# Kernel optimization log

Measured on AMD Instinct MI355X. Metric: run time of the kernel, lower is better.

Reference implementation:

```python
import jax, jax.numpy as jnp
import numpy as np

E = 16      # num_experts
K = 4       # num_experts_per_tok
H = 2048    # hidden_size
I = 1408    # moe_intermediate_size
SI = 5632   # shared expert intermediate size
CAP = 1024
NORM_TOPK = False


def setup_inputs() -> dict:
    key = jax.random.key(0)
    ks = jax.random.split(key, 9)
    def w(k, shape, fan_in):
        return jax.random.normal(k, shape, jnp.float32) * (fan_in ** -0.5)
    return {
        "hidden_states": jax.random.normal(ks[0], (1, 2048, H), jnp.float32),
        "gate_w":  w(ks[1], (E, H), H),        # router: Linear(H -> E), no bias
        "we_gate": w(ks[2], (E, I, H), H),     # per-expert gate_proj weights
        "we_up":   w(ks[3], (E, I, H), H),     # per-expert up_proj weights
        "we_down": w(ks[4], (E, H, I), I),     # per-expert down_proj weights
        "ws_gate": w(ks[5], (SI, H), H),       # shared expert gate_proj
        "ws_up":   w(ks[6], (SI, H), H),       # shared expert up_proj
        "ws_down": w(ks[7], (H, SI), SI),      # shared expert down_proj
        "sg_w":    w(ks[8], (1, H), H),        # shared_expert_gate: Linear(H -> 1)
    }


def reference(hidden_states, gate_w, we_gate, we_up, we_down,
              ws_gate, ws_up, ws_down, sg_w):
    B, S, Hd = hidden_states.shape
    x = hidden_states.reshape(-1, Hd)                      # [T, H]
    T = x.shape[0]

    # --- router ---
    router_logits = x @ gate_w.T                           # [T, E]
    probs = jax.nn.softmax(router_logits.astype(jnp.float32), axis=-1)
    topw, topi = jax.lax.top_k(probs, K)                   # [T, K]
    if NORM_TOPK:
        topw = topw / topw.sum(axis=-1, keepdims=True)

    # --- dispatch: flatten (token, slot) assignments ---
    A = T * K
    fe = topi.reshape(A)                                   # expert id per assignment
    fw = topw.reshape(A)                                   # routing weight per assignment
    ft = jnp.repeat(jnp.arange(T), K)                      # token id per assignment
    # position of each assignment within its expert (rank in arrival order)
    oh = jax.nn.one_hot(fe, E, dtype=jnp.int32)            # [A, E]
    pos = jnp.take_along_axis(jnp.cumsum(oh, axis=0) - 1, fe[:, None], axis=1)[:, 0]
    valid = pos < CAP
    # scatter tokens into per-expert buffers; overflow goes to dummy row CAP
    buf = jnp.zeros((E, CAP + 1, Hd), x.dtype)
    buf = buf.at[fe, jnp.where(valid, pos, CAP)].set(x[ft])[:, :CAP]  # [E, C, H]

    # --- per-expert SiLU-gated MLP (batched grouped GEMMs) ---
    g = jnp.einsum('ech,eih->eci', buf, we_gate)
    u = jnp.einsum('ech,eih->eci', buf, we_up)
    eo = jnp.einsum('eci,ehi->ech', jax.nn.silu(g) * u, we_down)      # [E, C, H]

    # --- combine: weighted scatter-add back to tokens ---
    ga = eo[fe, jnp.minimum(pos, CAP - 1)]                 # [A, H]
    wcomb = (fw * valid.astype(fw.dtype)).astype(x.dtype)
    y = jnp.zeros((T, Hd), x.dtype).at[ft].add(ga * wcomb[:, None])

    # --- shared expert with sigmoid gate ---
    sh = (jax.nn.silu(x @ ws_gate.T) * (x @ ws_up.T)) @ ws_down.T
    sh = jax.nn.sigmoid(x @ sg_w.T) * sh

    out = (y + sh).reshape(B, S, Hd)
    return out, router_logits
```

## Files before the change

kernel.cpp:

```cpp
#include <hip/hip_runtime.h>

#define T_TOK 2048
#define NE 16
#define KTOP 4
#define HD 2048
#define ID 1408
#define SID 5632
#define CAPACITY 1024

typedef __attribute__((ext_vector_type(8))) short short8;
typedef __attribute__((ext_vector_type(4))) float floatx4;

__device__ __forceinline__ short f2b(float f){
  union { float f; unsigned u; } v; v.f = f;
  unsigned r = v.u + 0x7fffu + ((v.u >> 16) & 1u);
  return (short)(r >> 16);
}
__device__ __forceinline__ float b2f(short s){
  union { float f; unsigned u; } v; v.u = ((unsigned)(unsigned short)s) << 16;
  return v.f;
}
__device__ __forceinline__ unsigned cvt_pk(float a, float b){
  unsigned r;
  asm("v_cvt_pk_bf16_f32 %0, %1, %2" : "=v"(r) : "v"(a), "v"(b));
  return r;
}
__device__ __forceinline__ short8 cvt8(float4 a, float4 b){
  union { unsigned d[4]; short8 s; } u;
  u.d[0] = cvt_pk(a.x, a.y); u.d[1] = cvt_pk(a.z, a.w);
  u.d[2] = cvt_pk(b.x, b.y); u.d[3] = cvt_pk(b.z, b.w);
  return u.s;
}
__device__ __forceinline__ void gl16(const void* g, void* l){
  __builtin_amdgcn_global_load_lds(
      (const __attribute__((address_space(1))) void*)g,
      (__attribute__((address_space(3))) void*)l, 16, 0, 0);
}

__device__ __forceinline__ void conv_range(
    int cb, int ncb,
    const float* __restrict__ s1, short* __restrict__ d1, long long n1,
    const float* __restrict__ s2, short* __restrict__ d2, long long n2)
{
  const long long tot = n1 + n2;
  const long long stride = (long long)ncb * 256;
  #pragma unroll 2
  for (long long i = (long long)cb * 256 + threadIdx.x; i < tot; i += stride){
    const float* s; short8* d; long long j;
    if (i < n1){ s = s1; d = (short8*)d1; j = i; }
    else       { s = s2; d = (short8*)d2; j = i - n1; }
    float4 f0 = ((const float4*)s)[j * 2];
    float4 f1 = ((const float4*)s)[j * 2 + 1];
    d[j] = cvt8(f0, f1);
  }
}

__global__ void moe_zero(int* __restrict__ counts){
  if (threadIdx.x < NE) counts[threadIdx.x] = 0;
}

__global__ void moe_router(const float* __restrict__ x,
                           const float* __restrict__ gate_w,
                           const float* __restrict__ sg_w,
                           float* __restrict__ logits_out,
                           short* __restrict__ xb,
                           int* __restrict__ counts,
                           int* __restrict__ slot_token,
                           float* __restrict__ slot_w,
                           int* __restrict__ tslot,
                           float* __restrict__ tw,
                           float* __restrict__ sg,
                           const float* cs1, short* cd1, long long cn1,
                           const float* cs2, short* cd2, long long cn2)
{
  if (blockIdx.x >= 512){
    conv_range(blockIdx.x - 512, gridDim.x - 512, cs1, cd1, cn1, cs2, cd2, cn2);
    return;
  }
  int wave = threadIdx.x >> 6, lane = threadIdx.x & 63;
  int t = (blockIdx.x << 2) + wave;
  const float4* xr = (const float4*)(x + (size_t)t * HD);
  short8* xbw = (short8*)(xb + (size_t)t * HD);
  float acc[17];
  #pragma unroll
  for (int e = 0; e < 17; ++e) acc[e] = 0.f;
  #pragma unroll
  for (int j = 0; j < 4; ++j){
    int i4 = (j * 64 + lane) * 2;
    float4 x0 = xr[i4], x1 = xr[i4 + 1];
    xbw[j * 64 + lane] = cvt8(x0, x1);
    #pragma unroll
    for (int e = 0; e < 16; ++e){
      const float4* gr = (const float4*)(gate_w + e * HD);
      float4 g0 = gr[i4], g1 = gr[i4 + 1];
      acc[e] += x0.x*g0.x + x0.y*g0.y + x0.z*g0.z + x0.w*g0.w
              + x1.x*g1.x + x1.y*g1.y + x1.z*g1.z + x1.w*g1.w;
    }
    const float4* sr = (const float4*)sg_w;
    float4 s0 = sr[i4], s1 = sr[i4 + 1];
    acc[16] += x0.x*s0.x + x0.y*s0.y + x0.z*s0.z + x0.w*s0.w
             + x1.x*s1.x + x1.y*s1.y + x1.z*s1.z + x1.w*s1.w;
  }
  #pragma unroll
  for (int e = 0; e < 17; ++e){
    float v = acc[e];
    #pragma unroll
    for (int off = 32; off > 0; off >>= 1) v += __shfl_xor(v, off, 64);
    acc[e] = v;
  }
  if (lane == 0){
    float m = acc[0];
    #pragma unroll
    for (int e = 1; e < 16; ++e) m = fmaxf(m, acc[e]);
    float p[16]; float s = 0.f;
    #pragma unroll
    for (int e = 0; e < 16; ++e){ p[e] = expf(acc[e] - m); s += p[e]; }
    float inv = 1.f / s;
    #pragma unroll
    for (int e = 0; e < 16; ++e) logits_out[t * 16 + e] = acc[e];
    unsigned used = 0;
    for (int k = 0; k < KTOP; ++k){
      float best = -1.f; int bi = 0;
      #pragma unroll
      for (int e = 0; e < 16; ++e){
        float pe = ((used >> e) & 1u) ? -1.f : p[e];
        if (pe > best){ best = pe; bi = e; }
      }
      used |= (1u << bi);
      int pos = atomicAdd(&counts[bi], 1);
      int enc = -1;
      if (pos < CAPACITY){
        slot_token[bi * CAPACITY + pos] = t;
        slot_w[bi * CAPACITY + pos] = best * inv;
        enc = bi * CAPACITY + pos;
      }
      tslot[t * KTOP + k] = enc;
      tw[t * KTOP + k] = best * inv;
    }
    sg[t] = 1.f / (1.f + expf(-acc[16]));
  }
}


#define GEMM_PREAMBLE \
  const int tid = threadIdx.x; \
  const int lane = tid & 63, wave = tid >> 6; \
  const int wr = wave >> 1, wc = wave & 1; \
  const int lrow = lane & 15, lk = lane >> 4; \
  const int s_th = (tid & 7) ^ ((tid >> 3) & 7); \
  const int koff = (s_th & 3) << 3; \
  const int rloc = ((tid >> 3) << 1) + (s_th >> 2); \
  const int lb = lrow >> 1; \
  const int soff = (((((lrow & 1) << 2) | lk) ^ (lb & 7)) << 4); \
  const int abase = (wr * 32 + lb) * 128 + soff;

__global__ __launch_bounds__(256) void moe_gateup(
    const short* __restrict__ Asrc,
    const short* __restrict__ Wg, const short* __restrict__ Wu,
    short* __restrict__ Out,
    const int* __restrict__ counts, const int* __restrict__ slot_token,
    int Ndim, int Kdim, int expert_mode, int mtiles, int ntiles,
    const float* cs1, short* cd1, long long cn1,
    const float* cs2, short* cd2, long long cn2, int conv_nwg)
{
  if ((int)blockIdx.x < conv_nwg){
    conv_range(blockIdx.x, conv_nwg, cs1, cd1, cn1, cs2, cd2, cn2);
    return;
  }
  int nwg = gridDim.x - conv_nwg;
  int bid = blockIdx.x - conv_nwg;
  int wg = ((bid & 7) * (nwg >> 3)) + (bid >> 3);
  int m_t = wg % mtiles; wg /= mtiles;
  int n_t = wg % ntiles; int e = wg / ntiles;

  int cnt = T_TOK; size_t woff = 0; short* out = Out;
  if (expert_mode){
    cnt = counts[e]; if (cnt > CAPACITY) cnt = CAPACITY;
    if (m_t * 128 >= cnt) return;
    woff = (size_t)e * Ndim * Kdim;
    out = Out + (size_t)e * CAPACITY * Ndim;
  }
  const int m0 = m_t * 128, n0 = n_t * 64;

  __shared__ __align__(16) char smem[2][16384];

  GEMM_PREAMBLE
  const int gbase = 8192 + (wc * 16 + lb) * 128 + soff;

  const short* aP[2];
  #pragma unroll
  for (int i = 0; i < 2; ++i){
    int p = m0 + i * 64 + rloc;
    const short* base;
    if (expert_mode){
      int q = (p < cnt) ? p : 0;
      base = Asrc + (size_t)slot_token[e * CAPACITY + q] * Kdim;
    } else base = Asrc + (size_t)p * Kdim;
    aP[i] = base + koff;
  }
  const short* bgP = Wg + woff + (size_t)(n0 + rloc) * Kdim + koff;
  const short* buP = Wu + woff + (size_t)(n0 + rloc) * Kdim + koff;

  const floatx4 vzero = {0.f, 0.f, 0.f, 0.f};
  floatx4 accg[4][2], accu[4][2];
  #pragma unroll
  for (int i = 0; i < 4; ++i)
    #pragma unroll
    for (int j = 0; j < 2; ++j){ accg[i][j] = vzero; accu[i][j] = vzero; }

#define GU_STAGE(B, K) { char* _b = smem[B]; \
    gl16(aP[0] + (K), _b + tid * 16); \
    gl16(aP[1] + (K), _b + 4096 + tid * 16); \
    gl16(bgP + (K),   _b + 8192 + tid * 16); \
    gl16(buP + (K),   _b + 12288 + tid * 16); }

#define GU_COMPUTE(B) { const char* bb = smem[B]; \
    short8 a[4], bg[2], bu[2]; \
    _Pragma("unroll") \
    for (int mf = 0; mf < 4; ++mf) a[mf] = *(const short8*)(bb + abase + mf * 1024); \
    _Pragma("unroll") \
    for (int nf = 0; nf < 2; ++nf){ \
      bg[nf] = *(const short8*)(bb + gbase + nf * 1024); \
      bu[nf] = *(const short8*)(bb + gbase + 4096 + nf * 1024); } \
    _Pragma("unroll") \
    for (int mf = 0; mf < 4; ++mf) \
      _Pragma("unroll") \
      for (int nf = 0; nf < 2; ++nf){ \
        accg[mf][nf] = __builtin_amdgcn_mfma_f32_16x16x32_bf16(a[mf], bg[nf], accg[mf][nf], 0, 0, 0); \
        accu[mf][nf] = __builtin_amdgcn_mfma_f32_16x16x32_bf16(a[mf], bu[nf], accu[mf][nf], 0, 0, 0); } }

  const int NSTEP = Kdim >> 5;
  GU_STAGE(0, 0)
  int cur = 0;
  for (int s = 0; s < NSTEP - 1; ++s){
    GU_STAGE(cur ^ 1, (s + 1) << 5)
    asm volatile("s_waitcnt vmcnt(4)" ::: "memory");
    asm volatile("s_barrier" ::: "memory");
    GU_COMPUTE(cur)
    asm volatile("s_barrier" ::: "memory");
    cur ^= 1;
  }
  asm volatile("s_waitcnt vmcnt(0)" ::: "memory");
  asm volatile("s_barrier" ::: "memory");
  GU_COMPUTE(cur)

  const int colbase = n0 + wc * 32 + lrow;
  #pragma unroll
  for (int mf = 0; mf < 4; ++mf){
    int pr = m0 + wr * 64 + mf * 16 + lk * 4;
    #pragma unroll
    for (int nf = 0; nf < 2; ++nf){
      floatx4 g4 = accg[mf][nf], u4 = accu[mf][nf];
      int col = colbase + nf * 16;
      #pragma unroll
      for (int r = 0; r < 4; ++r){
        float gv = g4[r], uv = u4[r];
        float a = (gv / (1.f + __expf(-gv))) * uv;
        out[(size_t)(pr + r) * Ndim + col] = f2b(a);
      }
    }
  }
}

template<int NF>
__global__ __launch_bounds__(256) void moe_down(
    const short* __restrict__ Asrc, const short* __restrict__ Wd,
    float* __restrict__ y, short* __restrict__ eo,
    const int* __restrict__ counts, const int* __restrict__ slot_token,
    const float* __restrict__ slot_w, const float* __restrict__ sgate,
    int Kdim, int expert_mode, int mtiles, int ntiles)
{
  int nwg = gridDim.x;
  int wg = ((blockIdx.x & 7) * (nwg >> 3)) + (blockIdx.x >> 3);
  int m_t = wg % mtiles; wg /= mtiles;
  int n_t = wg % ntiles; int e = wg / ntiles;

  int cnt = T_TOK; const short* ab = Asrc; size_t woff = 0;
  if (expert_mode){
    cnt = counts[e]; if (cnt > CAPACITY) cnt = CAPACITY;
    if (m_t * 128 >= cnt) return;
    ab = Asrc + (size_t)e * CAPACITY * Kdim;
    woff = (size_t)e * HD * Kdim;
  }
  const int m0 = m_t * 128, n0 = n_t * (NF * 32);

  __shared__ __align__(16) char smem[2][8192 + NF * 2048];

  GEMM_PREAMBLE
  const int bbase = 8192 + (wc * (NF * 8) + lb) * 128 + soff;

  const short* aP[2];
  #pragma unroll
  for (int i = 0; i < 2; ++i)
    aP[i] = ab + (size_t)(m0 + i * 64 + rloc) * Kdim + koff;
  const short* bP[NF / 2];
  #pragma unroll
  for (int i = 0; i < NF / 2; ++i)
    bP[i] = Wd + woff + (size_t)(n0 + i * 64 + rloc) * Kdim + koff;

  const floatx4 vzero = {0.f, 0.f, 0.f, 0.f};
  floatx4 acc[4][NF];
  #pragma unroll
  for (int i = 0; i < 4; ++i)
    #pragma unroll
    for (int j = 0; j < NF; ++j) acc[i][j] = vzero;

#define DN_STAGE(B, K) { char* _b = smem[B]; \
    gl16(aP[0] + (K), _b + tid * 16); \
    gl16(aP[1] + (K), _b + 4096 + tid * 16); \
    _Pragma("unroll") \
    for (int i = 0; i < NF / 2; ++i) \
      gl16(bP[i] + (K), _b + 8192 + i * 4096 + tid * 16); }

#define DN_COMPUTE(B) { const char* bb = smem[B]; \
    short8 a[4], b[NF]; \
    _Pragma("unroll") \
    for (int mf = 0; mf < 4; ++mf) a[mf] = *(const short8*)(bb + abase + mf * 1024); \
    _Pragma("unroll") \
    for (int nf = 0; nf < NF; ++nf) b[nf] = *(const short8*)(bb + bbase + nf * 1024); \
    _Pragma("unroll") \
    for (int mf = 0; mf < 4; ++mf) \
      _Pragma("unroll") \
      for (int nf = 0; nf < NF; ++nf) \
        acc[mf][nf] = __builtin_amdgcn_mfma_f32_16x16x32_bf16(a[mf], b[nf], acc[mf][nf], 0, 0, 0); }

  const int NSTEP = Kdim >> 5;
  DN_STAGE(0, 0)
  int cur = 0;
  for (int s = 0; s < NSTEP - 1; ++s){
    DN_STAGE(cur ^ 1, (s + 1) << 5)
    if (NF == 4) asm volatile("s_waitcnt vmcnt(4)" ::: "memory");
    else         asm volatile("s_waitcnt vmcnt(3)" ::: "memory");
    asm volatile("s_barrier" ::: "memory");
    DN_COMPUTE(cur)
    asm volatile("s_barrier" ::: "memory");
    cur ^= 1;
  }
  asm volatile("s_waitcnt vmcnt(0)" ::: "memory");
  asm volatile("s_barrier" ::: "memory");
  DN_COMPUTE(cur)

  const int colb = n0 + wc * (NF * 16) + lrow;
  if (expert_mode){
    #pragma unroll
    for (int mf = 0; mf < 4; ++mf){
      int pr = m0 + wr * 64 + mf * 16 + lk * 4;
      #pragma unroll
      for (int r = 0; r < 4; ++r){
        int p = pr + r;
        #pragma unroll
        for (int nf = 0; nf < NF; ++nf)
          eo[(size_t)(e * CAPACITY + p) * HD + colb + nf * 16] = f2b(acc[mf][nf][r]);
      }
    }
  } else {
    #pragma unroll
    for (int mf = 0; mf < 4; ++mf){
      int pr = m0 + wr * 64 + mf * 16 + lk * 4;
      #pragma unroll
      for (int r = 0; r < 4; ++r){
        int t = pr + r;
        float sv = sgate[t];
        #pragma unroll
        for (int nf = 0; nf < NF; ++nf)
          y[(size_t)t * HD + colb + nf * 16] = sv * acc[mf][nf][r];
      }
    }
  }
}

__global__ void moe_combine(const short* __restrict__ eo,
                            const int* __restrict__ tslot,
                            const float* __restrict__ tw,
                            float* __restrict__ y)
{
  int t = blockIdx.x;
  int o = threadIdx.x << 3;
  float* yp = y + (size_t)t * HD + o;
  float4 a0 = *(const float4*)yp, a1 = *(const float4*)(yp + 4);
  float acc[8] = {a0.x, a0.y, a0.z, a0.w, a1.x, a1.y, a1.z, a1.w};
  #pragma unroll
  for (int k = 0; k < KTOP; ++k){
    int s = tslot[t * KTOP + k];
    if (s >= 0){
      float w = tw[t * KTOP + k];
      short8 v = *(const short8*)(eo + (size_t)s * HD + o);
      #pragma unroll
      for (int j = 0; j < 8; ++j) acc[j] += w * b2f(v[j]);
    }
  }
  float4 r0 = {acc[0], acc[1], acc[2], acc[3]};
  float4 r1 = {acc[4], acc[5], acc[6], acc[7]};
  *(float4*)yp = r0; *(float4*)(yp + 4) = r1;
}

extern "C" void kernel_launch(void* const* d_in, const int* in_sizes, int n_in,
                              void* d_out, int out_size, void* d_ws, size_t ws_size,
                              hipStream_t stream)
{
  (void)in_sizes; (void)n_in; (void)out_size; (void)ws_size;
  const float* x       = (const float*)d_in[0];
  const float* gate_w  = (const float*)d_in[1];
  const float* we_gate = (const float*)d_in[2];
  const float* we_up   = (const float*)d_in[3];
  const float* we_down = (const float*)d_in[4];
  const float* wsg     = (const float*)d_in[5];
  const float* wsu     = (const float*)d_in[6];
  const float* wsd     = (const float*)d_in[7];
  const float* sg_w    = (const float*)d_in[8];

  float* y      = (float*)d_out;
  float* logits = y + (size_t)T_TOK * HD;

  const size_t N_EW = (size_t)NE * ID * HD;
  const size_t N_SW = (size_t)SID * HD;
  const long long G_EW = (long long)(N_EW / 8);
  const long long G_SW = (long long)(N_SW / 8);

  char* ws = (char*)d_ws;
  size_t off = 0;
  short* xb   = (short*)(ws + off); off += (size_t)T_TOK * HD * 2;
  short* wb   = (short*)(ws + off); off += (3 * N_EW + 3 * N_SW) * 2;
  short* act  = (short*)(ws + off); off += (size_t)NE * CAPACITY * ID * 2;
  short* acts = (short*)(ws + off); off += (size_t)T_TOK * SID * 2;
  int*   slot_token = (int*)  (ws + off); off += 65536;
  float* slot_w     = (float*)(ws + off); off += 65536;
  int*   tslot      = (int*)  (ws + off); off += 32768;
  float* tw         = (float*)(ws + off); off += 32768;
  int*   counts     = (int*)  (ws + off); off += 256;
  float* sg         = (float*)(ws + off);

  short* wbeg = wb;
  short* wbeu = wb + N_EW;
  short* wbed = wb + 2 * N_EW;
  short* wbsg = wb + 3 * N_EW;
  short* wbsu = wb + 3 * N_EW + N_SW;
  short* wbsd = wb + 3 * N_EW + 2 * N_SW;
  short* eo = wbeg;

  moe_zero<<<1, 64, 0, stream>>>(counts);
  moe_router<<<512 + 512, 256, 0, stream>>>(x, gate_w, sg_w, logits, xb,
                                            counts, slot_token, slot_w, tslot, tw, sg,
                                            wsg, wbsg, G_SW, wsu, wbsu, G_SW);
  moe_gateup<<<512 + 16 * 88, 256, 0, stream>>>(xb, wbsg, wbsu, acts,
                                                nullptr, nullptr, SID, HD, 0, 16, 88,
                                                we_gate, wbeg, G_EW, we_up, wbeu, G_EW, 512);
  moe_gateup<<<512 + 8 * 22 * NE, 256, 0, stream>>>(xb, wbeg, wbeu, act,
                                                    counts, slot_token, ID, HD, 1, 8, 22,
                                                    we_down, wbed, G_EW, wsd, wbsd, G_SW, 512);
  moe_down<2><<<16 * 32, 256, 0, stream>>>(acts, wbsd, y, nullptr, nullptr, nullptr,
                                           nullptr, sg, SID, 0, 16, 32);
  moe_down<4><<<8 * 16 * NE, 256, 0, stream>>>(act, wbed, y, eo, counts, slot_token,
                                               slot_w, nullptr, ID, 1, 8, 16);
  moe_combine<<<T_TOK, 256, 0, stream>>>(eo, tslot, tw, y);
}
```

Measured before the change: 797.4 us.

## Use triple-buffered LDS pipeline with two-step-ahead prefetch in MoE GEMMs

Both the gate/up and down GEMM kernels go from double-buffered to triple-buffered shared memory. Global loads are issued two K-steps ahead, and the vmcnt waits are adjusted so more memory latency is hidden behind the MFMA work. The unused slot_w routing-weight array and its writes are also removed. The larger LDS footprint (48KB per block for gateup) may reduce the number of resident workgroups per CU.

```diff
diff --git a/kernel.cpp b/kernel.cpp
--- a/kernel.cpp
+++ b/kernel.cpp
@@ -66,7 +66,6 @@
                            short* __restrict__ xb,
                            int* __restrict__ counts,
                            int* __restrict__ slot_token,
-                           float* __restrict__ slot_w,
                            int* __restrict__ tslot,
                            float* __restrict__ tw,
                            float* __restrict__ sg,
@@ -131,7 +130,6 @@
       int enc = -1;
       if (pos < CAPACITY){
         slot_token[bi * CAPACITY + pos] = t;
-        slot_w[bi * CAPACITY + pos] = best * inv;
         enc = bi * CAPACITY + pos;
       }
       tslot[t * KTOP + k] = enc;
@@ -154,6 +152,13 @@
   const int soff = (((((lrow & 1) << 2) | lk) ^ (lb & 7)) << 4); \
   const int abase = (wr * 32 + lb) * 128 + soff;
 
+#define WAIT8  asm volatile("s_waitcnt vmcnt(8)" ::: "memory");
+#define WAIT6  asm volatile("s_waitcnt vmcnt(6)" ::: "memory");
+#define WAIT4  asm volatile("s_waitcnt vmcnt(4)" ::: "memory");
+#define WAIT3  asm volatile("s_waitcnt vmcnt(3)" ::: "memory");
+#define WAIT0  asm volatile("s_waitcnt vmcnt(0)" ::: "memory");
+#define SBAR   asm volatile("s_barrier" ::: "memory");
+
 __global__ __launch_bounds__(256) void moe_gateup(
     const short* __restrict__ Asrc,
     const short* __restrict__ Wg, const short* __restrict__ Wu,
@@ -182,21 +187,23 @@
   }
   const int m0 = m_t * 128, n0 = n_t * 64;
 
-  __shared__ __align__(16) char smem[2][16384];
+  __shared__ __align__(16) char smem[3][16384];
 
   GEMM_PREAMBLE
   const int gbase = 8192 + (wc * 16 + lb) * 128 + soff;
 
-  const short* aP[2];
-  #pragma unroll
-  for (int i = 0; i < 2; ++i){
-    int p = m0 + i * 64 + rloc;
-    const short* base;
+  const short* aP0;
+  const short* aP1;
+  {
+    int p0 = m0 + rloc, p1 = m0 + 64 + rloc;
     if (expert_mode){
-      int q = (p < cnt) ? p : 0;
-      base = Asrc + (size_t)slot_token[e * CAPACITY + q] * Kdim;
-    } else base = Asrc + (size_t)p * Kdim;
-    aP[i] = base + koff;
+      int q0 = (p0 < cnt) ? p0 : 0, q1 = (p1 < cnt) ? p1 : 0;
+      aP0 = Asrc + (size_t)slot_token[e * CAPACITY + q0] * Kdim + koff;
+      aP1 = Asrc + (size_t)slot_token[e * CAPACITY + q1] * Kdim + koff;
+    } else {
+      aP0 = Asrc + (size_t)p0 * Kdim + koff;
+      aP1 = Asrc + (size_t)p1 * Kdim + koff;
+    }
   }
   const short* bgP = Wg + woff + (size_t)(n0 + rloc) * Kdim + koff;
   const short* buP = Wu + woff + (size_t)(n0 + rloc) * Kdim + koff;
@@ -208,13 +215,13 @@
     #pragma unroll
     for (int j = 0; j < 2; ++j){ accg[i][j] = vzero; accu[i][j] = vzero; }
 
-#define GU_STAGE(B, K) { char* _b = smem[B]; \
-    gl16(aP[0] + (K), _b + tid * 16); \
-    gl16(aP[1] + (K), _b + 4096 + tid * 16); \
-    gl16(bgP + (K),   _b + 8192 + tid * 16); \
-    gl16(buP + (K),   _b + 12288 + tid * 16); }
-
-#define GU_COMPUTE(B) { const char* bb = smem[B]; \
+#define GU_ISSUE(B, T) { char* _b = (B); const int _k = (T) << 5; \
+    gl16(aP0 + _k, _b + tid * 16); \
+    gl16(aP1 + _k, _b + 4096 + tid * 16); \
+    gl16(bgP + _k, _b + 8192 + tid * 16); \
+    gl16(buP + _k, _b + 12288 + tid * 16); }
+
+#define GU_COMPUTE(B) { const char* bb = (B); \
     short8 a[4], bg[2], bu[2]; \
     _Pragma("unroll") \
     for (int mf = 0; mf < 4; ++mf) a[mf] = *(const short8*)(bb + abase + mf * 1024); \
@@ -230,19 +237,20 @@
         accu[mf][nf] = __builtin_amdgcn_mfma_f32_16x16x32_bf16(a[mf], bu[nf], accu[mf][nf], 0, 0, 0); } }
 
   const int NSTEP = Kdim >> 5;
-  GU_STAGE(0, 0)
-  int cur = 0;
-  for (int s = 0; s < NSTEP - 1; ++s){
-    GU_STAGE(cur ^ 1, (s + 1) << 5)
-    asm volatile("s_waitcnt vmcnt(4)" ::: "memory");
-    asm volatile("s_barrier" ::: "memory");
-    GU_COMPUTE(cur)
-    asm volatile("s_barrier" ::: "memory");
-    cur ^= 1;
-  }
-  asm volatile("s_waitcnt vmcnt(0)" ::: "memory");
-  asm volatile("s_barrier" ::: "memory");
-  GU_COMPUTE(cur)
+  char* b0 = smem[0];
+  char* b1 = smem[1];
+  char* b2 = smem[2];
+  GU_ISSUE(b0, 0)
+  GU_ISSUE(b1, 1)
+  for (int s = 0; s < NSTEP; ++s){
+    if (s + 2 < NSTEP){ GU_ISSUE(b2, s + 2) WAIT8 }
+    else if (s + 2 == NSTEP){ WAIT4 }
+    else { WAIT0 }
+    SBAR
+    GU_COMPUTE(b0)
+    SBAR
+    char* t = b0; b0 = b1; b1 = b2; b2 = t;
+  }
 
   const int colbase = n0 + wc * 32 + lrow;
   #pragma unroll
@@ -267,7 +275,7 @@
     const short* __restrict__ Asrc, const short* __restrict__ Wd,
     float* __restrict__ y, short* __restrict__ eo,
     const int* __restrict__ counts, const int* __restrict__ slot_token,
-    const float* __restrict__ slot_w, const float* __restrict__ sgate,
+    const float* __restrict__ sgate,
     int Kdim, int expert_mode, int mtiles, int ntiles)
 {
   int nwg = gridDim.x;
@@ -284,19 +292,15 @@
   }
   const int m0 = m_t * 128, n0 = n_t * (NF * 32);
 
-  __shared__ __align__(16) char smem[2][8192 + NF * 2048];
+  __shared__ __align__(16) char smem[3][8192 + NF * 2048];
 
   GEMM_PREAMBLE
   const int bbase = 8192 + (wc * (NF * 8) + lb) * 128 + soff;
 
-  const short* aP[2];
-  #pragma unroll
-  for (int i = 0; i < 2; ++i)
-    aP[i] = ab + (size_t)(m0 + i * 64 + rloc) * Kdim + koff;
-  const short* bP[NF / 2];
-  #pragma unroll
-  for (int i = 0; i < NF / 2; ++i)
-    bP[i] = Wd + woff + (size_t)(n0 + i * 64 + rloc) * Kdim + koff;
+  const short* aP0 = ab + (size_t)(m0 + rloc) * Kdim + koff;
+  const short* aP1 = ab + (size_t)(m0 + 64 + rloc) * Kdim + koff;
+  const short* bP0 = Wd + woff + (size_t)(n0 + rloc) * Kdim + koff;
+  const short* bP1 = (NF == 4) ? (Wd + woff + (size_t)(n0 + 64 + rloc) * Kdim + koff) : bP0;
 
   const floatx4 vzero = {0.f, 0.f, 0.f, 0.f};
   floatx4 acc[4][NF];
@@ -305,14 +309,13 @@
     #pragma unroll
     for (int j = 0; j < NF; ++j) acc[i][j] = vzero;
 
-#define DN_STAGE(B, K) { char* _b = smem[B]; \
-    gl16(aP[0] + (K), _b + tid * 16); \
-    gl16(aP[1] + (K), _b + 4096 + tid * 16); \
-    _Pragma("unroll") \
-    for (int i = 0; i < NF / 2; ++i) \
-      gl16(bP[i] + (K), _b + 8192 + i * 4096 + tid * 16); }
-
-#define DN_COMPUTE(B) { const char* bb = smem[B]; \
+#define DN_ISSUE(B, T) { char* _b = (B); const int _k = (T) << 5; \
+    gl16(aP0 + _k, _b + tid * 16); \
+    gl16(aP1 + _k, _b + 4096 + tid * 16); \
+    gl16(bP0 + _k, _b + 8192 + tid * 16); \
+    if (NF == 4) gl16(bP1 + _k, _b + 12288 + tid * 16); }
+
+#define DN_COMPUTE(B) { const char* bb = (B); \
     short8 a[4], b[NF]; \
     _Pragma("unroll") \
     for (int mf = 0; mf < 4; ++mf) a[mf] = *(const short8*)(bb + abase + mf * 1024); \
@@ -325,20 +328,23 @@
         acc[mf][nf] = __builtin_amdgcn_mfma_f32_16x16x32_bf16(a[mf], b[nf], acc[mf][nf], 0, 0, 0); }
 
   const int NSTEP = Kdim >> 5;
-  DN_STAGE(0, 0)
-  int cur = 0;
-  for (int s = 0; s < NSTEP - 1; ++s){
-    DN_STAGE(cur ^ 1, (s + 1) << 5)
-    if (NF == 4) asm volatile("s_waitcnt vmcnt(4)" ::: "memory");
-    else         asm volatile("s_waitcnt vmcnt(3)" ::: "memory");
-    asm volatile("s_barrier" ::: "memory");
-    DN_COMPUTE(cur)
-    asm volatile("s_barrier" ::: "memory");
-    cur ^= 1;
-  }
-  asm volatile("s_waitcnt vmcnt(0)" ::: "memory");
-  asm volatile("s_barrier" ::: "memory");
-  DN_COMPUTE(cur)
+  char* b0 = smem[0];
+  char* b1 = smem[1];
+  char* b2 = smem[2];
+  DN_ISSUE(b0, 0)
+  DN_ISSUE(b1, 1)
+  for (int s = 0; s < NSTEP; ++s){
+    if (s + 2 < NSTEP){
+      DN_ISSUE(b2, s + 2)
+      if (NF == 4){ WAIT8 } else { WAIT6 }
+    } else if (s + 2 == NSTEP){
+      if (NF == 4){ WAIT4 } else { WAIT3 }
+    } else { WAIT0 }
+    SBAR
+    DN_COMPUTE(b0)
+    SBAR
+    char* t = b0; b0 = b1; b1 = b2; b2 = t;
+  }
 
   const int colb = n0 + wc * (NF * 16) + lrow;
   if (expert_mode){
@@ -424,7 +430,6 @@
   short* act  = (short*)(ws + off); off += (size_t)NE * CAPACITY * ID * 2;
   short* acts = (short*)(ws + off); off += (size_t)T_TOK * SID * 2;
   int*   slot_token = (int*)  (ws + off); off += 65536;
-  float* slot_w     = (float*)(ws + off); off += 65536;
   int*   tslot      = (int*)  (ws + off); off += 32768;
   float* tw         = (float*)(ws + off); off += 32768;
   int*   counts     = (int*)  (ws + off); off += 256;
@@ -440,7 +445,7 @@
 
   moe_zero<<<1, 64, 0, stream>>>(counts);
   moe_router<<<512 + 512, 256, 0, stream>>>(x, gate_w, sg_w, logits, xb,
-                                            counts, slot_token, slot_w, tslot, tw, sg,
+                                            counts, slot_token, tslot, tw, sg,
                                             wsg, wbsg, G_SW, wsu, wbsu, G_SW);
   moe_gateup<<<512 + 16 * 88, 256, 0, stream>>>(xb, wbsg, wbsu, acts,
                                                 nullptr, nullptr, SID, HD, 0, 16, 88,
@@ -449,8 +454,8 @@
                                                     counts, slot_token, ID, HD, 1, 8, 22,
                                                     we_down, wbed, G_EW, wsd, wbsd, G_SW, 512);
   moe_down<2><<<16 * 32, 256, 0, stream>>>(acts, wbsd, y, nullptr, nullptr, nullptr,
-                                           nullptr, sg, SID, 0, 16, 32);
+                                           sg, SID, 0, 16, 32);
   moe_down<4><<<8 * 16 * NE, 256, 0, stream>>>(act, wbed, y, eo, counts, slot_token,
-                                               slot_w, nullptr, ID, 1, 8, 16);
+                                               nullptr, ID, 1, 8, 16);
   moe_combine<<<T_TOK, 256, 0, stream>>>(eo, tslot, tw, y);
 }
```

After: 759.6 us. 1.05x faster.
